# Kernel tuning notes

Hardware: AMD Instinct MI355X
Metric: run time of the kernel (lower is better)

## Reference

```python
import jax, jax.numpy as jnp
import numpy as np
import math

EMBED = 256
HEADS = 8
LEVELS = 4
POINTS = 4
HEAD_DIM = EMBED // HEADS
SHAPES = np.array([[128, 128], [64, 64], [32, 32], [16, 16]], dtype=np.int32)  # (H_l, W_l)


def setup_inputs() -> dict:
    key = jax.random.key(0)
    ks = jax.random.split(key, 8)
    B, N = 2, 10000
    M = int((SHAPES[:, 0] * SHAPES[:, 1]).sum())  # 21760
    query = jax.random.normal(ks[0], (B, N, EMBED), jnp.float32)
    key_t = jax.random.normal(ks[1], (B, M, EMBED), jnp.float32)
    value = jax.random.normal(ks[2], (B, M, EMBED), jnp.float32)
    ref_points = jax.random.uniform(ks[3], (B, N, 1, 2), jnp.float32)  # normalized [0,1]
    spatial_shapes = jnp.asarray(SHAPES)
    starts = np.concatenate([[0], np.cumsum(SHAPES[:, 0] * SHAPES[:, 1])[:-1]]).astype(np.int32)
    level_start_idx = jnp.asarray(starts)
    # sampling_offsets bias: the radial grid init from _reset_parameters
    thetas = np.arange(HEADS, dtype=np.float32) * (2.0 * math.pi / HEADS)
    grid = np.stack([np.cos(thetas), np.sin(thetas)], -1)
    grid = grid / np.abs(grid).max(-1, keepdims=True)
    grid = np.tile(grid[:, None, None, :], (1, LEVELS, POINTS, 1))
    grid = grid * (np.arange(POINTS, dtype=np.float32) + 1.0)[None, None, :, None]
    b_off = jnp.asarray(grid.reshape(-1), jnp.float32)
    W_off = 0.01 * jax.random.normal(ks[4], (EMBED, HEADS * LEVELS * POINTS * 2), jnp.float32)
    W_attn = 0.01 * jax.random.normal(ks[5], (EMBED, HEADS * LEVELS * POINTS), jnp.float32)
    b_attn = jnp.zeros((HEADS * LEVELS * POINTS,), jnp.float32)
    W_v = jax.random.normal(ks[6], (EMBED, EMBED), jnp.float32) / math.sqrt(EMBED)
    b_v = jnp.zeros((EMBED,), jnp.float32)
    return {"query": query, "key": key_t, "value": value, "ref_points": ref_points,
            "spatial_shapes": spatial_shapes, "level_start_idx": level_start_idx,
            "W_off": W_off, "b_off": b_off, "W_attn": W_attn, "b_attn": b_attn,
            "W_v": W_v, "b_v": b_v}


def reference(query, key, value, ref_points, spatial_shapes, level_start_idx,
              W_off, b_off, W_attn, b_attn, W_v, b_v):
    B, N, _ = query.shape
    # value projection, split into heads: (B, M, H, Dh)
    v = (value @ W_v + b_v).reshape(B, -1, HEADS, HEAD_DIM)
    # sampling offsets: (B, N, H, L, P, 2)
    off = (query @ W_off + b_off).reshape(B, N, HEADS, LEVELS, POINTS, 2)
    # attention weights: softmax over L*P
    aw = jax.nn.softmax((query @ W_attn + b_attn).reshape(B, N, HEADS, LEVELS * POINTS), axis=-1)
    aw = aw.reshape(B, N, HEADS, LEVELS, POINTS)
    shapes = np.asarray(spatial_shapes)  # static level shapes
    # normalize offsets per level: x by W_l, y by H_l
    wh = jnp.asarray(shapes[:, ::-1].astype(np.float32))  # (L, 2) = (W, H)
    off = off / wh[None, None, None, :, None, :]
    # K=1 reference point per query -> broadcast add
    locs = ref_points.reshape(B, N, 1, 1, 1, 2) + off  # (B, N, H, L, P, 2) in [0,1]
    starts = np.concatenate([[0], np.cumsum(shapes[:, 0] * shapes[:, 1])])
    b_idx = jnp.arange(B)[:, None, None, None]
    h_idx = jnp.arange(HEADS)[None, None, :, None]
    out = jnp.zeros((B, N, HEADS, HEAD_DIM), v.dtype)
    for l in range(LEVELS):
        Hl, Wl = int(shapes[l, 0]), int(shapes[l, 1])
        v_l = jax.lax.dynamic_slice_in_dim(v, int(starts[l]), Hl * Wl, axis=1)  # (B, Hl*Wl, H, Dh)
        loc = locs[:, :, :, l]  # (B, N, H, P, 2)
        # grid_sample semantics: grid = 2*loc - 1, align_corners=False, zero padding
        x = loc[..., 0] * Wl - 0.5
        y = loc[..., 1] * Hl - 0.5
        x0 = jnp.floor(x)
        y0 = jnp.floor(y)
        lx = x - x0
        ly = y - y0
        x0i = x0.astype(jnp.int32)
        y0i = y0.astype(jnp.int32)
        samp = jnp.zeros(x.shape + (HEAD_DIM,), v.dtype)  # (B, N, H, P, Dh)
        for dy, dx, w in ((0, 0, (1 - lx) * (1 - ly)), (0, 1, lx * (1 - ly)),
                          (1, 0, (1 - lx) * ly), (1, 1, lx * ly)):
            xi = x0i + dx
            yi = y0i + dy
            valid = (xi >= 0) & (xi < Wl) & (yi >= 0) & (yi < Hl)
            idx = jnp.clip(yi, 0, Hl - 1) * Wl + jnp.clip(xi, 0, Wl - 1)
            g = v_l[b_idx, idx, h_idx]  # per-head gather -> (B, N, H, P, Dh)
            samp = samp + jnp.where(valid, w, 0.0)[..., None] * g
        out = out + jnp.einsum('bnhpd,bnhp->bnhd', samp, aw[:, :, :, l])
    return out.reshape(B, N, EMBED)
```

## Files before the change

kernel.cpp:

```cpp
#include <hip/hip_runtime.h>
#include <hip/hip_bf16.h>

#define EMBED    256
#define HEADS    8
#define LEVELS   4
#define POINTS   4
#define BATCH    2
#define M_TOT    21760
#define LDP      (EMBED + 4)

typedef __hip_bfloat16 bf16;
typedef __attribute__((ext_vector_type(8))) short short8;
typedef __attribute__((ext_vector_type(8))) short bf16x8s;
typedef __attribute__((ext_vector_type(4))) float f32x4;

__device__ __constant__ int c_H[LEVELS]  = {128, 64, 32, 16};
__device__ __constant__ int c_St[LEVELS] = {0, 16384, 20480, 21504};

template<bool BF>
__device__ __forceinline__ float ldf(const void* p, size_t i) {
  if (BF) return __bfloat162float(((const bf16*)p)[i]);
  else    return ((const float*)p)[i];
}
__device__ __forceinline__ float vt2f(float x) { return x; }
__device__ __forceinline__ float vt2f(bf16 x)  { return __bfloat162float(x); }

__device__ __forceinline__ void stout(float* p, float v) { *p = v; }
__device__ __forceinline__ void stout(bf16* p, float v)  { *p = __float2bfloat16(v); }
__device__ __forceinline__ void stout_nt(float* p, float v) {
  __builtin_nontemporal_store(v, p);
}
__device__ __forceinline__ void stout_nt(bf16* p, float v)  { *p = __float2bfloat16(v); }

__device__ __forceinline__ void ld2c(const bf16* p, float& lo, float& hi) {
  unsigned u = *(const unsigned*)p;
  lo = __uint_as_float(u << 16);
  hi = __uint_as_float(u & 0xFFFF0000u);
}
__device__ __forceinline__ void ld2c(const float* p, float& lo, float& hi) {
  float2 f = *(const float2*)p;
  lo = f.x; hi = f.y;
}

template<bool BF>
__device__ __forceinline__ float4 ld4(const void* p, size_t i) {
  if (BF) {
    ushort4 u = *(const ushort4*)((const bf16*)p + i);
// ... 16 lines not shown
}

__device__ __forceinline__ void split8(const f32x4 x, const f32x4 y,
                                       bf16x8s& h, bf16x8s& l) {
  float f[8] = {x[0], x[1], x[2], x[3], y[0], y[1], y[2], y[3]};
#pragma unroll
  for (int j = 0; j < 8; ++j) {
    bf16 hb = __float2bfloat16(f[j]);
    float r = f[j] - __bfloat162float(hb);
    bf16 lb = __float2bfloat16(r);
    h[j] = *reinterpret_cast<short*>(&hb);
    l[j] = *reinterpret_cast<short*>(&lb);
  }
}

__global__ __launch_bounds__(256)
void k_detect(const unsigned short* __restrict__ q16, int* __restrict__ flag) {
  __shared__ int cnt;
  if (threadIdx.x == 0) cnt = 0;
  __syncthreads();
  int c = 0;
  for (int i = threadIdx.x; i < 8192; i += 256) {
    unsigned short v = q16[i];
    if ((v & 0x7F80u) == 0x7F80u) ++c;
  }
  if (c) atomicAdd(&cnt, c);
  __syncthreads();
  if (threadIdx.x == 0) flag[0] = (cnt == 0) ? 1 : 0;
}

__global__ __launch_bounds__(256)
void k_transpose_bf16(const unsigned short* __restrict__ W,
                      unsigned short* __restrict__ WT,
                      int K, int N, const int* __restrict__ flag) {
  if (*flag != 1) return;
  __shared__ unsigned short tile[64][65];
  const int ntn = N >> 6;
  const int tk = (int)blockIdx.x / ntn;
  const int tn = (int)blockIdx.x % ntn;
  const int k0 = tk << 6, n0 = tn << 6;
  const int t   = threadIdx.x;
  const int row = t >> 2;
  const int cq  = (t & 3) << 4;
  const unsigned short* src = W + (size_t)(k0 + row) * N + n0 + cq;
#pragma unroll
  for (int j = 0; j < 16; ++j) tile[row][cq + j] = src[j];
  __syncthreads();
  unsigned short* dst = WT + (size_t)(n0 + row) * K + k0 + cq;
#pragma unroll
  for (int j = 0; j < 16; ++j) dst[j] = tile[cq + j][row];
}

__global__ __launch_bounds__(256)
void k_wsplit_all(const float* __restrict__ Wv, const float* __restrict__ Woff,
                  const float* __restrict__ Wattn,
                  bf16* __restrict__ Tvh, bf16* __restrict__ Tvl,
                  bf16* __restrict__ Toh, bf16* __restrict__ Tol,
                  bf16* __restrict__ Tah, bf16* __restrict__ Tal,
                  const int* __restrict__ flag) {
  if (*flag != 0) return;
  int bid = (int)blockIdx.x;
  const float* W; bf16 *H, *L; int N;
  if (bid < 16)      { W = Wv;    H = Tvh; L = Tvl; N = 256; }
  else if (bid < 32) { W = Woff;  H = Toh; L = Tol; N = 256; bid -= 16; }
  else               { W = Wattn; H = Tah; L = Tal; N = 128; bid -= 32; }
  const int K = 256;
  __shared__ float tile[64][65];
  const int ntn = N >> 6;
  const int tk = bid / ntn, tn = bid % ntn;
  const int k0 = tk << 6, n0 = tn << 6;
  const int t   = threadIdx.x;
  const int row = t >> 2;
  const int cq  = (t & 3) << 4;
  const float* src = W + (size_t)(k0 + row) * N + n0 + cq;
#pragma unroll
  for (int j = 0; j < 16; ++j) tile[row][cq + j] = src[j];
  __syncthreads();
  const size_t d0 = (size_t)(n0 + row) * K + k0 + cq;
#pragma unroll
  for (int j = 0; j < 16; ++j) {
    float v = tile[cq + j][row];
    bf16 hb = __float2bfloat16(v);
    float r = v - __bfloat162float(hb);
    H[d0 + j] = hb;
    L[d0 + j] = __float2bfloat16(r);
  }
}

template<class OT>
__global__ __launch_bounds__(256)
void k_mfma_proj(const bf16* __restrict__ A, const bf16* __restrict__ WT,
                 const void* __restrict__ bias, OT* __restrict__ C,
                 int M, int N, const int* __restrict__ flag) {
  if (*flag != 1) return;
  const int colBlocks = N >> 7;
  const int rb = (int)blockIdx.x / colBlocks;
  const int cb = (int)blockIdx.x % colBlocks;
  const int t   = threadIdx.x;
  const int wid = t >> 6;
  const int l   = t & 63;
  const int lrow = l & 15;
  const int lk8  = (l >> 4) << 3;
  const int r0 = rb * 64 + (wid & 1) * 32;
  const int c0 = cb * 128 + (wid >> 1) * 64;

  f32x4 acc[2][4];
#pragma unroll
  for (int rf = 0; rf < 2; ++rf)
#pragma unroll
    for (int cf = 0; cf < 4; ++cf) acc[rf][cf] = (f32x4){0.f, 0.f, 0.f, 0.f};

  const bf16* Ap0 = A + (size_t)min(r0 + lrow,      M - 1) * EMBED + lk8;
// ... 16 lines not shown
    acc[1][1] = __builtin_amdgcn_mfma_f32_16x16x32_bf16(a1, b1, acc[1][1], 0, 0, 0);
    acc[1][2] = __builtin_amdgcn_mfma_f32_16x16x32_bf16(a1, b2, acc[1][2], 0, 0, 0);
    acc[1][3] = __builtin_amdgcn_mfma_f32_16x16x32_bf16(a1, b3, acc[1][3], 0, 0, 0);
  }

  const int rbase = (l >> 4) << 2;
#pragma unroll
  for (int cf = 0; cf < 4; ++cf) {
    const int col = c0 + cf * 16 + lrow;
    const float bv = ldf<true>(bias, col);
#pragma unroll
    for (int rf = 0; rf < 2; ++rf) {
#pragma unroll
      for (int r = 0; r < 4; ++r) {
        const int row = r0 + rf * 16 + rbase + r;
        if (row < M) stout(&C[(size_t)row * N + col], acc[rf][cf][r] + bv);
      }
    }
  }
}

template<int NW, class OT>
__global__ __launch_bounds__(256)
void k_mfma_projf2(const float* __restrict__ A, const bf16* __restrict__ WThi,
                   const bf16* __restrict__ WTlo, const float* __restrict__ bias,
                   OT* __restrict__ C, int M, const int* __restrict__ flag) {
  if (*flag != 0) return;
  constexpr int N = NW * 64;
  const int t   = threadIdx.x;
  const int wid = t >> 6;
  const int l   = t & 63;
  const int lrow = l & 15;
  const int lk8  = (l >> 4) << 3;
  const int r0 = (int)blockIdx.x * 32;
  const int c0 = wid * 64;

  __shared__ float As[32][260];

  constexpr int RPW = 32 / NW;
#pragma unroll
  for (int base = 0; base < RPW; base += 8) {
    f32x4 tmp[8];
#pragma unroll
    for (int i = 0; i < 8; ++i) {
      int r   = wid + (base + i) * NW;
      int row = min(r0 + r, M - 1);
      tmp[i] = __builtin_nontemporal_load(
                 (const f32x4*)(A + (size_t)row * EMBED + (l << 2)));
    }
#pragma unroll
    for (int i = 0; i < 8; ++i) {
      int r = wid + (base + i) * NW;
      *(f32x4*)&As[r][l << 2] = tmp[i];
    }
  }
  __syncthreads();

  f32x4 acc[2][4];
#pragma unroll
  for (int rf = 0; rf < 2; ++rf)
#pragma unroll
    for (int cf = 0; cf < 4; ++cf) acc[rf][cf] = (f32x4){0.f, 0.f, 0.f, 0.f};

  const bf16* Bh = WThi + (size_t)(c0 + lrow) * EMBED + lk8;
  const bf16* Bl = WTlo + (size_t)(c0 + lrow) * EMBED + lk8;

#pragma unroll
  for (int ks = 0; ks < 8; ++ks) {
    const int k = ks * 32;
    bf16x8s a0h, a0l, a1h, a1l;
    split8(*(const f32x4*)&As[lrow     ][k + lk8],
           *(const f32x4*)&As[lrow     ][k + lk8 + 4], a0h, a0l);
    split8(*(const f32x4*)&As[lrow + 16][k + lk8],
           *(const f32x4*)&As[lrow + 16][k + lk8 + 4], a1h, a1l);
    bf16x8s bh0 = *(const bf16x8s*)(Bh + 0 * 16 * EMBED + k);
    bf16x8s bh1 = *(const bf16x8s*)(Bh + 1 * 16 * EMBED + k);
    bf16x8s bh2 = *(const bf16x8s*)(Bh + 2 * 16 * EMBED + k);
    bf16x8s bh3 = *(const bf16x8s*)(Bh + 3 * 16 * EMBED + k);
    bf16x8s bl0 = *(const bf16x8s*)(Bl + 0 * 16 * EMBED + k);
    bf16x8s bl1 = *(const bf16x8s*)(Bl + 1 * 16 * EMBED + k);
// ... 23 lines not shown
    acc[1][1] = __builtin_amdgcn_mfma_f32_16x16x32_bf16(a1l, bh1, acc[1][1], 0, 0, 0);
    acc[1][2] = __builtin_amdgcn_mfma_f32_16x16x32_bf16(a1l, bh2, acc[1][2], 0, 0, 0);
    acc[1][3] = __builtin_amdgcn_mfma_f32_16x16x32_bf16(a1l, bh3, acc[1][3], 0, 0, 0);
  }

  const int rbase = (l >> 4) << 2;
#pragma unroll
  for (int cf = 0; cf < 4; ++cf) {
    const int col = c0 + cf * 16 + lrow;
    const float bv = bias[col];
#pragma unroll
    for (int rf = 0; rf < 2; ++rf) {
#pragma unroll
      for (int r = 0; r < 4; ++r) {
        const int row = r0 + rf * 16 + rbase + r;
        if (row < M) stout_nt(&C[(size_t)row * N + col], acc[rf][cf][r] + bv);
      }
    }
  }
}

template<bool BF>
__device__ __forceinline__ void stage16(const void* __restrict__ A,
                                        float (*rowA)[LDP],
                                        int r0, int M, int t) {
  int r  = t >> 4;
  int rr = min(r0 + r, M - 1);
  int c0 = (t & 15) * 16;
  if (BF) {
    const bf16* ap = (const bf16*)A + (size_t)rr * EMBED + c0;
    short8 a0 = *(const short8*)ap;
// ... 128 lines not shown
template<bool BF, class VT>
__device__ void fused2_body(const void* __restrict__ ref_points,
                            const float* __restrict__ off_pre,
                            const float* __restrict__ scores,
                            const VT* __restrict__ v,
                            void* __restrict__ out, int N, int BN) {
  int q = blockIdx.x;
  if (q >= BN) return;
  int b = q / N;
  int t = threadIdx.x;

  __shared__ float  s_aw[128];
  __shared__ float  s_rp[2];
  __shared__ int4   s_pi[128];
  __shared__ float4 s_pw[128];
  __shared__ float  s_part[2][256];

  if (t < 2)   s_rp[t] = ldf<BF>(ref_points, (size_t)q * 2 + t);
  if (t < 128) s_aw[t] = __builtin_nontemporal_load(&scores[(size_t)q * 128 + t]);
  __syncthreads();

  if (t < 128) {
    int base = t & ~15;
    float mx = -1e30f;
#pragma unroll
    for (int i = 0; i < 16; ++i) mx = fmaxf(mx, s_aw[base + i]);
    float sum = 0.f;
#pragma unroll
    for (int i = 0; i < 16; ++i) sum += expf(s_aw[base + i] - mx);
    float wa = expf(s_aw[t] - mx) / sum;

// ... 61 lines not shown
    oL0 = fmaf(wA.z, lA2, oL0); oH0 = fmaf(wA.z, hA2, oH0);
    oL1 = fmaf(wA.w, lA3, oL1); oH1 = fmaf(wA.w, hA3, oH1);
    oL0 = fmaf(wB.x, lB0, oL0); oH0 = fmaf(wB.x, hB0, oH0);
    oL1 = fmaf(wB.y, lB1, oL1); oH1 = fmaf(wB.y, hB1, oH1);
    oL0 = fmaf(wB.z, lB2, oL0); oH0 = fmaf(wB.z, hB2, oH0);
    oL1 = fmaf(wB.w, lB3, oL1); oH1 = fmaf(wB.w, hB3, oH1);
    oL0 = fmaf(wC.x, lC0, oL0); oH0 = fmaf(wC.x, hC0, oH0);
    oL1 = fmaf(wC.y, lC1, oL1); oH1 = fmaf(wC.y, hC1, oH1);
    oL0 = fmaf(wC.z, lC2, oL0); oH0 = fmaf(wC.z, hC2, oH0);
    oL1 = fmaf(wC.w, lC3, oL1); oH1 = fmaf(wC.w, hC3, oH1);
    oL0 = fmaf(wD.x, lD0, oL0); oH0 = fmaf(wD.x, hD0, oH0);
    oL1 = fmaf(wD.y, lD1, oL1); oH1 = fmaf(wD.y, hD1, oH1);
    oL0 = fmaf(wD.z, lD2, oL0); oH0 = fmaf(wD.z, hD2, oH0);
    oL1 = fmaf(wD.w, lD3, oL1); oH1 = fmaf(wD.w, hD3, oH1);
  }
  s_part[s][ch]     = oL0 + oL1;
  s_part[s][ch + 1] = oH0 + oH1;
  __syncthreads();

  float o = s_part[0][t] + s_part[1][t];
  if (BF) {
    bf16 ob = __float2bfloat16(o);
    __builtin_nontemporal_store(*reinterpret_cast<unsigned short*>(&ob),
                                (unsigned short*)out + (size_t)q * EMBED + t);
  } else {
    __builtin_nontemporal_store(o, (float*)out + (size_t)q * EMBED + t);
  }
}

template<class VT>
__global__ __launch_bounds__(256)
void k_fused2(const void* ref_points, const float* off_pre, const float* scores,
              const VT* v, void* out, int N, int BN, const int* flag) {
  if (*flag) fused2_body<true,  VT>(ref_points, off_pre, scores, v, out, N, BN);
  else       fused2_body<false, VT>(ref_points, off_pre, scores, v, out, N, BN);
}

template<bool BF>
__device__ void vgemv8_body(const void* __restrict__ A, const void* __restrict__ W,
                            const void* __restrict__ bias, float* __restrict__ C,
                            int M) {
  const int t  = threadIdx.x;
  const int r0 = blockIdx.x * 8;
  if (r0 >= M) return;

  __shared__ float rowA[8][EMBED];
  {
    int r  = t >> 5;
    int rr = min(r0 + r, M - 1);
    int c0 = (t & 31) * 8;
// ... 23 lines not shown
  for (int k = 0; k < EMBED; ++k) {
    float w = ldf<BF>(W, (size_t)k * EMBED + n);
#pragma unroll
    for (int r = 0; r < 8; ++r) acc[r] = fmaf(rowA[r][k], w, acc[r]);
  }
#pragma unroll
  for (int r = 0; r < 8; ++r)
    if (r0 + r < M) C[(size_t)(r0 + r) * EMBED + n] = acc[r];
}

__global__ __launch_bounds__(256)
void k_vgemv8(const void* A, const void* W, const void* bias, float* C,
              int M, const int* flag) {
  if (*flag) vgemv8_body<true >(A, W, bias, C, M);
  else       vgemv8_body<false>(A, W, bias, C, M);
}

template<bool BF, class VT>
__device__ void fused_body(const void* __restrict__ query,
                           const void* __restrict__ ref_points,
                           const float* __restrict__ off_pre,
                           const void* __restrict__ W_attn,
                           const void* __restrict__ b_attn,
                           const VT* __restrict__ v,
                           void* __restrict__ out, int N, int BN) {
  int q = blockIdx.x;
  if (q >= BN) return;
  int b = q / N;
  int t = threadIdx.x;

  __shared__ float  row[EMBED];
  __shared__ float  s_part[256];
  __shared__ float  s_aw[HEADS * LEVELS * POINTS];
  __shared__ float  s_rp[2];
  __shared__ int4   s_pi[HEADS * LEVELS * POINTS];
  __shared__ float4 s_pw[HEADS * LEVELS * POINTS];

  row[t] = ldf<BF>(query, (size_t)q * EMBED + t);
  if (t < 2) s_rp[t] = ldf<BF>(ref_points, (size_t)q * 2 + t);
  __syncthreads();

  {
    const int col = t & 127;
    const int e0  = (t >> 7) * 128;
    float acc = 0.f;
#pragma unroll 8
    for (int e = 0; e < 128; ++e)
      acc = fmaf(row[e0 + e], ldf<BF>(W_attn, (size_t)(e0 + e) * 128 + col), acc);
    s_part[t] = acc;
  }
  __syncthreads();
  if (t < 128)
    s_aw[t] = ldf<BF>(b_attn, t) + s_part[t] + s_part[t + 128];
  __syncthreads();

  if (t < 128) {
    int base = t & ~15;
    float mx = -1e30f;
#pragma unroll
    for (int i = 0; i < 16; ++i) mx = fmaxf(mx, s_aw[base + i]);
    float sum = 0.f;
#pragma unroll
    for (int i = 0; i < 16; ++i) sum += expf(s_aw[base + i] - mx);
    float wa = expf(s_aw[t] - mx) / sum;

    int   l  = (t >> 2) & 3;
    int   Wl = 128 >> l;
    float fW = (float)Wl;
    int   st = (int)((65536u - (65536u >> (2 * l))) / 3u);
    float ox = off_pre[(size_t)q * EMBED + 2 * t]     - 0.5f;
    float oy = off_pre[(size_t)q * EMBED + 2 * t + 1] - 0.5f;
    float x = fmaf(s_rp[0], fW, ox);
    float y = fmaf(s_rp[1], fW, oy);
    float x0f = floorf(x), y0f = floorf(y);
    float lx = x - x0f, ly = y - y0f;
    int x0 = (int)x0f, y0 = (int)y0f;
    int x1 = x0 + 1,   y1 = y0 + 1;
    float w00 = wa * (1.f - lx) * (1.f - ly);
    float w01 = wa * lx * (1.f - ly);
    float w10 = wa * (1.f - lx) * ly;
    float w11 = wa * lx * ly;
    bool vx0 = (unsigned)x0 < (unsigned)Wl;
    bool vx1 = (unsigned)x1 < (unsigned)Wl;
    bool vy0 = (unsigned)y0 < (unsigned)Wl;
    bool vy1 = (unsigned)y1 < (unsigned)Wl;
    int xc0 = min(max(x0, 0), Wl - 1), xc1 = min(max(x1, 0), Wl - 1);
    int yc0 = min(max(y0, 0), Wl - 1), yc1 = min(max(y1, 0), Wl - 1);
    int r0i = st + yc0 * Wl;
    int r1i = st + yc1 * Wl;
    int4 pi; float4 pw;
    pi.x = (r0i + xc0) << 8;  pw.x = (vx0 && vy0) ? w00 : 0.f;
    pi.y = (r0i + xc1) << 8;  pw.y = (vx1 && vy0) ? w01 : 0.f;
    pi.z = (r1i + xc0) << 8;  pw.z = (vx0 && vy1) ? w10 : 0.f;
    pi.w = (r1i + xc1) << 8;  pw.w = (vx1 && vy1) ? w11 : 0.f;
    s_pi[t] = pi;
    s_pw[t] = pw;
  }
  __syncthreads();

  const int h = t >> 5;
  const VT* vbt = v + (size_t)b * M_TOT * EMBED + t;
  float o = 0.f;
#pragma unroll
  for (int lp = 0; lp < 16; ++lp) {
    int c = (h << 4) + lp;
    int4   i4 = s_pi[c];
    float4 w4 = s_pw[c];
    o = fmaf(w4.x, vt2f(vbt[i4.x]), o);
    o = fmaf(w4.y, vt2f(vbt[i4.y]), o);
    o = fmaf(w4.z, vt2f(vbt[i4.z]), o);
    o = fmaf(w4.w, vt2f(vbt[i4.w]), o);
  }
  if (BF) ((bf16*)out)[(size_t)q * EMBED + t] = __float2bfloat16(o);
  else    ((float*)out)[(size_t)q * EMBED + t] = o;
}

template<class VT>
__global__ __launch_bounds__(256)
void k_fused(const void* query, const void* ref_points, const float* off_pre,
             const void* W_attn, const void* b_attn,
             const VT* v, void* out, int N, int BN, const int* flag) {
  if (*flag) fused_body<true,  VT>(query, ref_points, off_pre, W_attn, b_attn, v, out, N, BN);
  else       fused_body<false, VT>(query, ref_points, off_pre, W_attn, b_attn, v, out, N, BN);
}

template<bool BF, class VT>
__device__ void vproj_body(const void* __restrict__ value,
                           const void* __restrict__ W_v,
                           const void* __restrict__ b_v,
                           VT* __restrict__ v, int BM) {
  int m = blockIdx.x;
  if (m >= BM) return;
  int t = threadIdx.x;
  __shared__ float row[EMBED];
  row[t] = ldf<BF>(value, (size_t)m * EMBED + t);
  __syncthreads();
  float acc = ldf<BF>(b_v, t);
#pragma unroll 8
  for (int e = 0; e < EMBED; ++e)
    acc = fmaf(row[e], ldf<BF>(W_v, (size_t)e * EMBED + t), acc);
  if (sizeof(VT) == 2) ((bf16*)v)[(size_t)m * EMBED + t] = __float2bfloat16(acc);
  else                 ((float*)v)[(size_t)m * EMBED + t] = acc;
}

template<class VT>
__global__ __launch_bounds__(256)
void k_value_proj(const void* value, const void* W_v, const void* b_v,
                  VT* v, int BM, const int* flag) {
  if (*flag) vproj_body<true,  VT>(value, W_v, b_v, v, BM);
  else       vproj_body<false, VT>(value, W_v, b_v, v, BM);
}

template<bool BF, class VT>
__device__ void fusedfb_body(const void* __restrict__ query,
                             const void* __restrict__ ref_points,
                             const void* __restrict__ W_off,
                             const void* __restrict__ b_off,
                             const void* __restrict__ W_attn,
                             const void* __restrict__ b_attn,
                             const VT* __restrict__ v,
                             void* __restrict__ out, int N, int BN) {
  int q = blockIdx.x;
  if (q >= BN) return;
  int b = q / N;
  int t = threadIdx.x;
// ... 73 lines not shown
  }
  if (BF) ((bf16*)out)[(size_t)q * EMBED + t] = __float2bfloat16(o);
  else    ((float*)out)[(size_t)q * EMBED + t] = o;
}

template<class VT>
__global__ __launch_bounds__(256)
void k_fused_fb(const void* query, const void* ref_points,
                const void* W_off, const void* b_off,
                const void* W_attn, const void* b_attn,
                const VT* v, void* out, int N, int BN, const int* flag) {
  if (*flag) fusedfb_body<true,  VT>(query, ref_points, W_off, b_off, W_attn, b_attn, v, out, N, BN);
  else       fusedfb_body<false, VT>(query, ref_points, W_off, b_off, W_attn, b_attn, v, out, N, BN);
}

extern "C" void kernel_launch(void* const* d_in, const int* in_sizes, int n_in,
                              void* d_out, int out_size, void* d_ws, size_t ws_size,
                              hipStream_t stream) {
  const void* query      = d_in[0];
  const void* value      = d_in[2];
  const void* ref_points = d_in[3];
  const void* W_off  = d_in[6];
  const void* b_off  = d_in[7];
  const void* W_attn = d_in[8];
  const void* b_attn = d_in[9];
  const void* W_v    = d_in[10];
  const void* b_v    = d_in[11];

  const int BN = in_sizes[0] / EMBED;
  const int BM = in_sizes[2] / EMBED;
  const int N  = BN / BATCH;

  int*  flag    = (int*)d_ws;
  char* ws_base = (char*)d_ws + 256;

  k_detect<<<1, 256, 0, stream>>>((const unsigned short*)query, flag);

  const size_t sz_v    = (size_t)BM * EMBED * sizeof(float);
  const size_t sz_off  = (size_t)BN * EMBED * sizeof(float);
  const size_t sz_attn = (size_t)BN * 128 * sizeof(float);
  const size_t sz_T    = (size_t)(256 * 256 * 2 + 256 * 128) * 2  * 2;
  const size_t need_mfma = 256 + sz_v + sz_off + sz_attn + sz_T;
  const size_t need_full = 256 + sz_v + sz_off + sz_attn;
  const size_t need_mid  = 256 + sz_v + sz_off;

  if (ws_size >= need_mfma) {
    bf16*  ws_v    = (bf16*)ws_base;
    float* ws_off  = (float*)(ws_base + sz_v);
    float* ws_attn = (float*)(ws_base + sz_v + sz_off);
    unsigned short* wsT = (unsigned short*)(ws_base + sz_v + sz_off + sz_attn);
    unsigned short* wsT_v    = wsT;
    unsigned short* wsT_off  = wsT + 256 * 256;
    unsigned short* wsT_attn = wsT + 2 * 256 * 256;
    bf16* Tvh = (bf16*)wsT;
    bf16* Tvl = Tvh + 256 * 256;
    bf16* Toh = Tvl + 256 * 256;
    bf16* Tol = Toh + 256 * 256;
    bf16* Tah = Tol + 256 * 256;
    bf16* Tal = Tah + 256 * 128;

    const int rbV64 = (BM + 63) / 64;
    const int rbQ64 = (BN + 63) / 64;
    k_transpose_bf16<<<16, 256, 0, stream>>>((const unsigned short*)W_v,    wsT_v,    256, 256, flag);
    k_transpose_bf16<<<16, 256, 0, stream>>>((const unsigned short*)W_off,  wsT_off,  256, 256, flag);
    k_transpose_bf16<<< 8, 256, 0, stream>>>((const unsigned short*)W_attn, wsT_attn, 256, 128, flag);
    k_mfma_proj<bf16 ><<<rbV64 * 2, 256, 0, stream>>>((const bf16*)value, (const bf16*)wsT_v,
                                                      b_v, ws_v, BM, 256, flag);
    k_mfma_proj<float><<<rbQ64 * 2, 256, 0, stream>>>((const bf16*)query, (const bf16*)wsT_off,
                                                      b_off, ws_off, BN, 256, flag);
    k_mfma_proj<float><<<rbQ64,     256, 0, stream>>>((const bf16*)query, (const bf16*)wsT_attn,
                                                      b_attn, ws_attn, BN, 128, flag);

    const int gV32 = (BM + 31) / 32;
    const int gQ32 = (BN + 31) / 32;
    k_wsplit_all<<<40, 256, 0, stream>>>((const float*)W_v, (const float*)W_off,
                                         (const float*)W_attn,
                                         Tvh, Tvl, Toh, Tol, Tah, Tal, flag);
    k_mfma_projf2<4, bf16 ><<<gV32, 256, 0, stream>>>((const float*)value, Tvh, Tvl,
                                                      (const float*)b_v, ws_v, BM, flag);
    k_mfma_projf2<4, float><<<gQ32, 256, 0, stream>>>((const float*)query, Toh, Tol,
                                                      (const float*)b_off, ws_off, BN, flag);
    k_mfma_projf2<2, float><<<gQ32, 128, 0, stream>>>((const float*)query, Tah, Tal,
                                                      (const float*)b_attn, ws_attn, BN, flag);

    k_fused2<bf16><<<BN, 256, 0, stream>>>(ref_points, ws_off, ws_attn, ws_v,
                                           d_out, N, BN, flag);
  } else if (ws_size >= need_full) {
    float* ws_v    = (float*)ws_base;
    float* ws_off  = (float*)(ws_base + sz_v);
    float* ws_attn = (float*)(ws_base + sz_v + sz_off);
    k_vgemv4x4<<<(BM + 15) / 16, 256, 0, stream>>>(value, W_v, b_v, ws_v, BM, flag);
    k_vgemv4x4<<<(BN + 15) / 16, 256, 0, stream>>>(query, W_off, b_off, ws_off, BN, flag);
    k_agemv4<<<(BN + 15) / 16, 256, 0, stream>>>(query, W_attn, b_attn, ws_attn, BN, flag);
    k_fused2<float><<<BN, 256, 0, stream>>>(ref_points, ws_off, ws_attn, ws_v,
                                            d_out, N, BN, flag);
  } else if (ws_size >= need_mid) {
    float* ws_v   = (float*)ws_base;
    float* ws_off = (float*)(ws_base + sz_v);
    k_vgemv8<<<(BM + 7) / 8, 256, 0, stream>>>(value, W_v, b_v, ws_v, BM, flag);
    k_vgemv8<<<(BN + 7) / 8, 256, 0, stream>>>(query, W_off, b_off, ws_off, BN, flag);
    k_fused<float><<<BN, 256, 0, stream>>>(query, ref_points, ws_off,
                                           W_attn, b_attn, ws_v, d_out, N, BN, flag);
  } else {
    bf16* ws_v = (bf16*)ws_base;
    k_value_proj<bf16><<<BM, 256, 0, stream>>>(value, W_v, b_v, ws_v, BM, flag);
    k_fused_fb<bf16><<<BN, 256, 0, stream>>>(query, ref_points, W_off, b_off,
                                             W_attn, b_attn, ws_v, d_out, N, BN, flag);
  }
}
```

Before: 317.5 us.

## Merge detect/transpose/split and projection launches into fewer combined kernels

Folds dtype detection into an 80-block prep kernel that also performs the bf16 weight transpose or the fp32 hi/lo split, so every block detects redundantly and skips the branch it does not need. The three bf16 projection GEMMs and the three fp32 split-precision GEMMs each become a single launch that routes work segments by block index. This cuts the launch count from about eleven to four on the main path, reducing launch gaps and tail underutilisation. The cost is redundant detection reads in every prep block and idle waves in the attention segment, which now uses 256-thread blocks with half the waves exiting early. It also changes the fused kernel's partial-sum shared layout and removes the unused mid-size fallback path.

New measurement: 287.5 us. 1.1x faster.

```diff
diff --git a/kernel.cpp b/kernel.cpp
--- a/kernel.cpp
+++ b/kernel.cpp
@@ -27,10 +27,6 @@
 
 __device__ __forceinline__ void stout(float* p, float v) { *p = v; }
 __device__ __forceinline__ void stout(bf16* p, float v)  { *p = __float2bfloat16(v); }
-__device__ __forceinline__ void stout_nt(float* p, float v) {
-  __builtin_nontemporal_store(v, p);
-}
-__device__ __forceinline__ void stout_nt(bf16* p, float v)  { *p = __float2bfloat16(v); }
 
 __device__ __forceinline__ void ld2c(const bf16* p, float& lo, float& hi) {
   unsigned u = *(const unsigned*)p;
@@ -77,88 +73,111 @@
   }
 }
 
-__global__ __launch_bounds__(256)
-void k_detect(const unsigned short* __restrict__ q16, int* __restrict__ flag) {
-  __shared__ int cnt;
-  if (threadIdx.x == 0) cnt = 0;
+__device__ __forceinline__ int block_detect(const unsigned short* q16, int t,
+                                            int* cnt) {
+  if (t == 0) *cnt = 0;
   __syncthreads();
   int c = 0;
-  for (int i = threadIdx.x; i < 8192; i += 256) {
+  for (int i = t; i < 8192; i += 256) {
     unsigned short v = q16[i];
     if ((v & 0x7F80u) == 0x7F80u) ++c;
   }
-  if (c) atomicAdd(&cnt, c);
-  __syncthreads();
-  if (threadIdx.x == 0) flag[0] = (cnt == 0) ? 1 : 0;
+  if (c) atomicAdd(cnt, c);
+  __syncthreads();
+  return (*cnt == 0) ? 1 : 0;
 }
 
 __global__ __launch_bounds__(256)
-void k_transpose_bf16(const unsigned short* __restrict__ W,
-                      unsigned short* __restrict__ WT,
-                      int K, int N, const int* __restrict__ flag) {
-  if (*flag != 1) return;
-  __shared__ unsigned short tile[64][65];
-  const int ntn = N >> 6;
-  const int tk = (int)blockIdx.x / ntn;
-  const int tn = (int)blockIdx.x % ntn;
-  const int k0 = tk << 6, n0 = tn << 6;
-  const int t   = threadIdx.x;
+void k_prep(const unsigned short* __restrict__ q16, int* __restrict__ flag,
+            const void* __restrict__ Wv, const void* __restrict__ Woff,
+            const void* __restrict__ Wattn,
+            unsigned short* __restrict__ wsT_v,
+            unsigned short* __restrict__ wsT_off,
+            unsigned short* __restrict__ wsT_attn,
+            bf16* __restrict__ Tvh, bf16* __restrict__ Tvl,
+            bf16* __restrict__ Toh, bf16* __restrict__ Tol,
+            bf16* __restrict__ Tah, bf16* __restrict__ Tal) {
+  __shared__ int cnt;
+  __shared__ float  ftile[64][65];
+  __shared__ unsigned short stile[64][65];
+
+  const int t = threadIdx.x;
+  const int isbf = block_detect(q16, t, &cnt);
+  if ((int)blockIdx.x == 0 && t == 0) flag[0] = isbf;
+
   const int row = t >> 2;
   const int cq  = (t & 3) << 4;
-  const unsigned short* src = W + (size_t)(k0 + row) * N + n0 + cq;
-#pragma unroll
-  for (int j = 0; j < 16; ++j) tile[row][cq + j] = src[j];
-  __syncthreads();
-  unsigned short* dst = WT + (size_t)(n0 + row) * K + k0 + cq;
-#pragma unroll
-  for (int j = 0; j < 16; ++j) dst[j] = tile[cq + j][row];
+  const int K = 256;
+
+  if ((int)blockIdx.x < 40) {
+    if (isbf) return;
+    int bid = (int)blockIdx.x;
+    const float* W; bf16 *H, *L; int N;
+    if (bid < 16)      { W = (const float*)Wv;    H = Tvh; L = Tvl; N = 256; }
+    else if (bid < 32) { W = (const float*)Woff;  H = Toh; L = Tol; N = 256; bid -= 16; }
+    else               { W = (const float*)Wattn; H = Tah; L = Tal; N = 128; bid -= 32; }
+    const int ntn = N >> 6;
+    const int tk = bid / ntn, tn = bid % ntn;
+    const int k0 = tk << 6, n0 = tn << 6;
+    const float* src = W + (size_t)(k0 + row) * N + n0 + cq;
+#pragma unroll
+    for (int j = 0; j < 16; ++j) ftile[row][cq + j] = src[j];
+    __syncthreads();
+    const size_t d0 = (size_t)(n0 + row) * K + k0 + cq;
+#pragma unroll
+    for (int j = 0; j < 16; ++j) {
+      float v = ftile[cq + j][row];
+      bf16 hb = __float2bfloat16(v);
+      float r = v - __bfloat162float(hb);
+      H[d0 + j] = hb;
+      L[d0 + j] = __float2bfloat16(r);
+    }
+  } else {
+    if (!isbf) return;
+    int bid = (int)blockIdx.x - 40;
+    const unsigned short* W; unsigned short* WT; int N;
+    if (bid < 16)      { W = (const unsigned short*)Wv;    WT = wsT_v;    N = 256; }
+    else if (bid < 32) { W = (const unsigned short*)Woff;  WT = wsT_off;  N = 256; bid -= 16; }
+    else               { W = (const unsigned short*)Wattn; WT = wsT_attn; N = 128; bid -= 32; }
+    const int ntn = N >> 6;
+    const int tk = bid / ntn, tn = bid % ntn;
+    const int k0 = tk << 6, n0 = tn << 6;
+    const unsigned short* src = W + (size_t)(k0 + row) * N + n0 + cq;
+#pragma unroll
+    for (int j = 0; j < 16; ++j) stile[row][cq + j] = src[j];
+    __syncthreads();
+    unsigned short* dst = WT + (size_t)(n0 + row) * K + k0 + cq;
+#pragma unroll
+    for (int j = 0; j < 16; ++j) dst[j] = stile[cq + j][row];
+  }
 }
 
 __global__ __launch_bounds__(256)
-void k_wsplit_all(const float* __restrict__ Wv, const float* __restrict__ Woff,
-                  const float* __restrict__ Wattn,
-                  bf16* __restrict__ Tvh, bf16* __restrict__ Tvl,
-                  bf16* __restrict__ Toh, bf16* __restrict__ Tol,
-                  bf16* __restrict__ Tah, bf16* __restrict__ Tal,
-                  const int* __restrict__ flag) {
-  if (*flag != 0) return;
+void k_proj_all(const bf16* __restrict__ value, const bf16* __restrict__ query,
+                const unsigned short* __restrict__ wsT_v,
+                const unsigned short* __restrict__ wsT_off,
+                const unsigned short* __restrict__ wsT_attn,
+                const void* __restrict__ b_v, const void* __restrict__ b_off,
+                const void* __restrict__ b_attn,
+                bf16* __restrict__ Cv, float* __restrict__ Coff,
+                float* __restrict__ Cattn,
+                int BM, int BN, int g0, int g1,
+                const int* __restrict__ flag) {
+  if (*flag != 1) return;
   int bid = (int)blockIdx.x;
-  const float* W; bf16 *H, *L; int N;
-  if (bid < 16)      { W = Wv;    H = Tvh; L = Tvl; N = 256; }
-  else if (bid < 32) { W = Woff;  H = Toh; L = Tol; N = 256; bid -= 16; }
-  else               { W = Wattn; H = Tah; L = Tal; N = 128; bid -= 32; }
-  const int K = 256;
-  __shared__ float tile[64][65];
-  const int ntn = N >> 6;
-  const int tk = bid / ntn, tn = bid % ntn;
-  const int k0 = tk << 6, n0 = tn << 6;
-  const int t   = threadIdx.x;
-  const int row = t >> 2;
-  const int cq  = (t & 3) << 4;
-  const float* src = W + (size_t)(k0 + row) * N + n0 + cq;
-#pragma unroll
-  for (int j = 0; j < 16; ++j) tile[row][cq + j] = src[j];
-  __syncthreads();
-  const size_t d0 = (size_t)(n0 + row) * K + k0 + cq;
-#pragma unroll
-  for (int j = 0; j < 16; ++j) {
-    float v = tile[cq + j][row];
-    bf16 hb = __float2bfloat16(v);
-    float r = v - __bfloat162float(hb);
-    H[d0 + j] = hb;
-    L[d0 + j] = __float2bfloat16(r);
-  }
-}
-
-template<class OT>
-__global__ __launch_bounds__(256)
-void k_mfma_proj(const bf16* __restrict__ A, const bf16* __restrict__ WT,
-                 const void* __restrict__ bias, OT* __restrict__ C,
-                 int M, int N, const int* __restrict__ flag) {
-  if (*flag != 1) return;
+  int seg, sb;
+  if (bid < g0)            { seg = 0; sb = bid; }
+  else if (bid < g0 + g1)  { seg = 1; sb = bid - g0; }
+  else                     { seg = 2; sb = bid - g0 - g1; }
+
+  const bf16* A; const bf16* WT; const void* bias; int M, N;
+  if (seg == 0)      { A = value; WT = (const bf16*)wsT_v;    bias = b_v;    M = BM; N = 256; }
+  else if (seg == 1) { A = query; WT = (const bf16*)wsT_off;  bias = b_off;  M = BN; N = 256; }
+  else               { A = query; WT = (const bf16*)wsT_attn; bias = b_attn; M = BN; N = 128; }
+
   const int colBlocks = N >> 7;
-  const int rb = (int)blockIdx.x / colBlocks;
-  const int cb = (int)blockIdx.x % colBlocks;
+  const int rb = sb / colBlocks;
+  const int cb = sb % colBlocks;
   const int t   = threadIdx.x;
   const int wid = t >> 6;
   const int l   = t & 63;
@@ -205,56 +224,80 @@
 #pragma unroll
       for (int r = 0; r < 4; ++r) {
         const int row = r0 + rf * 16 + rbase + r;
-        if (row < M) stout(&C[(size_t)row * N + col], acc[rf][cf][r] + bv);
+        if (row < M) {
+          float o = acc[rf][cf][r] + bv;
+          size_t idx = (size_t)row * N + col;
+          if (seg == 0)      Cv[idx]   = __float2bfloat16(o);
+          else if (seg == 1) Coff[idx] = o;
+          else               Cattn[idx] = o;
+        }
       }
     }
   }
 }
 
-template<int NW, class OT>
 __global__ __launch_bounds__(256)
-void k_mfma_projf2(const float* __restrict__ A, const bf16* __restrict__ WThi,
-                   const bf16* __restrict__ WTlo, const float* __restrict__ bias,
-                   OT* __restrict__ C, int M, const int* __restrict__ flag) {
+void k_projf2_all(const float* __restrict__ value, const float* __restrict__ query,
+                  const bf16* __restrict__ Tvh, const bf16* __restrict__ Tvl,
+                  const bf16* __restrict__ Toh, const bf16* __restrict__ Tol,
+                  const bf16* __restrict__ Tah, const bf16* __restrict__ Tal,
+                  const float* __restrict__ b_v, const float* __restrict__ b_off,
+                  const float* __restrict__ b_attn,
+                  bf16* __restrict__ Cv, float* __restrict__ Coff,
+                  float* __restrict__ Cattn,
+                  int BM, int BN, int gV, int gQ,
+                  const int* __restrict__ flag) {
   if (*flag != 0) return;
-  constexpr int N = NW * 64;
+  int bid = (int)blockIdx.x;
+  int seg, rblk;
+  if (bid < gV)           { seg = 0; rblk = bid; }
+  else if (bid < gV + gQ) { seg = 1; rblk = bid - gV; }
+  else                    { seg = 2; rblk = bid - gV - gQ; }
+
+  const float* A; const bf16 *Bh0, *Bl0; const float* bias; int M, N;
+  if (seg == 0)      { A = value; Bh0 = Tvh; Bl0 = Tvl; bias = b_v;    M = BM; N = 256; }
+  else if (seg == 1) { A = query; Bh0 = Toh; Bl0 = Tol; bias = b_off;  M = BN; N = 256; }
+  else               { A = query; Bh0 = Tah; Bl0 = Tal; bias = b_attn; M = BN; N = 128; }
+
   const int t   = threadIdx.x;
   const int wid = t >> 6;
   const int l   = t & 63;
   const int lrow = l & 15;
   const int lk8  = (l >> 4) << 3;
-  const int r0 = (int)blockIdx.x * 32;
+  const int r0 = rblk * 32;
   const int c0 = wid * 64;
+  const bool active = (seg != 2) || (wid < 2);
 
   __shared__ float As[32][260];
 
-  constexpr int RPW = 32 / NW;
-#pragma unroll
-  for (int base = 0; base < RPW; base += 8) {
+#pragma unroll
+  for (int base = 0; base < 8; base += 8) {
     f32x4 tmp[8];
 #pragma unroll
     for (int i = 0; i < 8; ++i) {
-      int r   = wid + (base + i) * NW;
+      int r   = wid + (base + i) * 4;
       int row = min(r0 + r, M - 1);
       tmp[i] = __builtin_nontemporal_load(
                  (const f32x4*)(A + (size_t)row * EMBED + (l << 2)));
     }
 #pragma unroll
     for (int i = 0; i < 8; ++i) {
-      int r = wid + (base + i) * NW;
+      int r = wid + (base + i) * 4;
       *(f32x4*)&As[r][l << 2] = tmp[i];
     }
   }
   __syncthreads();
 
+  if (!active) return;
+
   f32x4 acc[2][4];
 #pragma unroll
   for (int rf = 0; rf < 2; ++rf)
 #pragma unroll
     for (int cf = 0; cf < 4; ++cf) acc[rf][cf] = (f32x4){0.f, 0.f, 0.f, 0.f};
 
-  const bf16* Bh = WThi + (size_t)(c0 + lrow) * EMBED + lk8;
-  const bf16* Bl = WTlo + (size_t)(c0 + lrow) * EMBED + lk8;
+  const bf16* Bh = Bh0 + (size_t)(c0 + lrow) * EMBED + lk8;
+  const bf16* Bl = Bl0 + (size_t)(c0 + lrow) * EMBED + lk8;
 
 #pragma unroll
   for (int ks = 0; ks < 8; ++ks) {
@@ -308,7 +351,13 @@
 #pragma unroll
       for (int r = 0; r < 4; ++r) {
         const int row = r0 + rf * 16 + rbase + r;
-        if (row < M) stout_nt(&C[(size_t)row * N + col], acc[rf][cf][r] + bv);
+        if (row < M) {
+          float o = acc[rf][cf][r] + bv;
+          size_t idx = (size_t)row * N + col;
+          if (seg == 0)      Cv[idx] = __float2bfloat16(o);
+          else if (seg == 1) __builtin_nontemporal_store(o, &Coff[idx]);
+          else               __builtin_nontemporal_store(o, &Cattn[idx]);
+        }
       }
     }
   }
@@ -467,7 +516,7 @@
   __shared__ float  s_rp[2];
   __shared__ int4   s_pi[128];
   __shared__ float4 s_pw[128];
-  __shared__ float  s_part[2][256];
+  __shared__ float  s_part[2][2][128];
 
   if (t < 2)   s_rp[t] = ldf<BF>(ref_points, (size_t)q * 2 + t);
   if (t < 128) s_aw[t] = __builtin_nontemporal_load(&scores[(size_t)q * 128 + t]);
@@ -559,11 +608,11 @@
     oL0 = fmaf(wD.z, lD2, oL0); oH0 = fmaf(wD.z, hD2, oH0);
     oL1 = fmaf(wD.w, lD3, oL1); oH1 = fmaf(wD.w, hD3, oH1);
   }
-  s_part[s][ch]     = oL0 + oL1;
-  s_part[s][ch + 1] = oH0 + oH1;
-  __syncthreads();
-
-  float o = s_part[0][t] + s_part[1][t];
+  s_part[s][0][c] = oL0 + oL1;
+  s_part[s][1][c] = oH0 + oH1;
+  __syncthreads();
+
+  float o = s_part[0][t & 1][t >> 1] + s_part[1][t & 1][t >> 1];
   if (BF) {
     bf16 ob = __float2bfloat16(o);
     __builtin_nontemporal_store(*reinterpret_cast<unsigned short*>(&ob),
@@ -579,6 +628,13 @@
               const VT* v, void* out, int N, int BN, const int* flag) {
   if (*flag) fused2_body<true,  VT>(ref_points, off_pre, scores, v, out, N, BN);
   else       fused2_body<false, VT>(ref_points, off_pre, scores, v, out, N, BN);
+}
+
+__global__ __launch_bounds__(256)
+void k_detect(const unsigned short* __restrict__ q16, int* __restrict__ flag) {
+  __shared__ int cnt;
+  int isbf = block_detect(q16, threadIdx.x, &cnt);
+  if (threadIdx.x == 0) flag[0] = isbf;
 }
 
 template<bool BF>
@@ -632,141 +688,6 @@
               int M, const int* flag) {
   if (*flag) vgemv8_body<true >(A, W, bias, C, M);
   else       vgemv8_body<false>(A, W, bias, C, M);
-}
-
-template<bool BF, class VT>
-__device__ void fused_body(const void* __restrict__ query,
-                           const void* __restrict__ ref_points,
-                           const float* __restrict__ off_pre,
-                           const void* __restrict__ W_attn,
-                           const void* __restrict__ b_attn,
-                           const VT* __restrict__ v,
-                           void* __restrict__ out, int N, int BN) {
-  int q = blockIdx.x;
-  if (q >= BN) return;
-  int b = q / N;
-  int t = threadIdx.x;
-
-  __shared__ float  row[EMBED];
-  __shared__ float  s_part[256];
-  __shared__ float  s_aw[HEADS * LEVELS * POINTS];
-  __shared__ float  s_rp[2];
-  __shared__ int4   s_pi[HEADS * LEVELS * POINTS];
-  __shared__ float4 s_pw[HEADS * LEVELS * POINTS];
-
-  row[t] = ldf<BF>(query, (size_t)q * EMBED + t);
-  if (t < 2) s_rp[t] = ldf<BF>(ref_points, (size_t)q * 2 + t);
-  __syncthreads();
-
-  {
-    const int col = t & 127;
-    const int e0  = (t >> 7) * 128;
-    float acc = 0.f;
-#pragma unroll 8
-    for (int e = 0; e < 128; ++e)
-      acc = fmaf(row[e0 + e], ldf<BF>(W_attn, (size_t)(e0 + e) * 128 + col), acc);
-    s_part[t] = acc;
-  }
-  __syncthreads();
-  if (t < 128)
-    s_aw[t] = ldf<BF>(b_attn, t) + s_part[t] + s_part[t + 128];
-  __syncthreads();
-
-  if (t < 128) {
-    int base = t & ~15;
-    float mx = -1e30f;
-#pragma unroll
-    for (int i = 0; i < 16; ++i) mx = fmaxf(mx, s_aw[base + i]);
-    float sum = 0.f;
-#pragma unroll
-    for (int i = 0; i < 16; ++i) sum += expf(s_aw[base + i] - mx);
-    float wa = expf(s_aw[t] - mx) / sum;
-
-    int   l  = (t >> 2) & 3;
-    int   Wl = 128 >> l;
-    float fW = (float)Wl;
-    int   st = (int)((65536u - (65536u >> (2 * l))) / 3u);
-    float ox = off_pre[(size_t)q * EMBED + 2 * t]     - 0.5f;
-    float oy = off_pre[(size_t)q * EMBED + 2 * t + 1] - 0.5f;
-    float x = fmaf(s_rp[0], fW, ox);
-    float y = fmaf(s_rp[1], fW, oy);
-    float x0f = floorf(x), y0f = floorf(y);
-    float lx = x - x0f, ly = y - y0f;
-    int x0 = (int)x0f, y0 = (int)y0f;
-    int x1 = x0 + 1,   y1 = y0 + 1;
-    float w00 = wa * (1.f - lx) * (1.f - ly);
-    float w01 = wa * lx * (1.f - ly);
-    float w10 = wa * (1.f - lx) * ly;
-    float w11 = wa * lx * ly;
-    bool vx0 = (unsigned)x0 < (unsigned)Wl;
-    bool vx1 = (unsigned)x1 < (unsigned)Wl;
-    bool vy0 = (unsigned)y0 < (unsigned)Wl;
-    bool vy1 = (unsigned)y1 < (unsigned)Wl;
-    int xc0 = min(max(x0, 0), Wl - 1), xc1 = min(max(x1, 0), Wl - 1);
-    int yc0 = min(max(y0, 0), Wl - 1), yc1 = min(max(y1, 0), Wl - 1);
-    int r0i = st + yc0 * Wl;
-    int r1i = st + yc1 * Wl;
-    int4 pi; float4 pw;
-    pi.x = (r0i + xc0) << 8;  pw.x = (vx0 && vy0) ? w00 : 0.f;
-    pi.y = (r0i + xc1) << 8;  pw.y = (vx1 && vy0) ? w01 : 0.f;
-    pi.z = (r1i + xc0) << 8;  pw.z = (vx0 && vy1) ? w10 : 0.f;
-    pi.w = (r1i + xc1) << 8;  pw.w = (vx1 && vy1) ? w11 : 0.f;
-    s_pi[t] = pi;
-    s_pw[t] = pw;
-  }
-  __syncthreads();
-
-  const int h = t >> 5;
-  const VT* vbt = v + (size_t)b * M_TOT * EMBED + t;
-  float o = 0.f;
-#pragma unroll
-  for (int lp = 0; lp < 16; ++lp) {
-    int c = (h << 4) + lp;
-    int4   i4 = s_pi[c];
-    float4 w4 = s_pw[c];
-    o = fmaf(w4.x, vt2f(vbt[i4.x]), o);
-    o = fmaf(w4.y, vt2f(vbt[i4.y]), o);
-    o = fmaf(w4.z, vt2f(vbt[i4.z]), o);
-    o = fmaf(w4.w, vt2f(vbt[i4.w]), o);
-  }
-  if (BF) ((bf16*)out)[(size_t)q * EMBED + t] = __float2bfloat16(o);
-  else    ((float*)out)[(size_t)q * EMBED + t] = o;
-}
-
-template<class VT>
-__global__ __launch_bounds__(256)
-void k_fused(const void* query, const void* ref_points, const float* off_pre,
-             const void* W_attn, const void* b_attn,
-             const VT* v, void* out, int N, int BN, const int* flag) {
-  if (*flag) fused_body<true,  VT>(query, ref_points, off_pre, W_attn, b_attn, v, out, N, BN);
-  else       fused_body<false, VT>(query, ref_points, off_pre, W_attn, b_attn, v, out, N, BN);
-}
-
-template<bool BF, class VT>
-__device__ void vproj_body(const void* __restrict__ value,
-                           const void* __restrict__ W_v,
-                           const void* __restrict__ b_v,
-                           VT* __restrict__ v, int BM) {
-  int m = blockIdx.x;
-  if (m >= BM) return;
-  int t = threadIdx.x;
-  __shared__ float row[EMBED];
-  row[t] = ldf<BF>(value, (size_t)m * EMBED + t);
-  __syncthreads();
-  float acc = ldf<BF>(b_v, t);
-#pragma unroll 8
-  for (int e = 0; e < EMBED; ++e)
-    acc = fmaf(row[e], ldf<BF>(W_v, (size_t)e * EMBED + t), acc);
-  if (sizeof(VT) == 2) ((bf16*)v)[(size_t)m * EMBED + t] = __float2bfloat16(acc);
-  else                 ((float*)v)[(size_t)m * EMBED + t] = acc;
-}
-
-template<class VT>
-__global__ __launch_bounds__(256)
-void k_value_proj(const void* value, const void* W_v, const void* b_v,
-                  VT* v, int BM, const int* flag) {
-  if (*flag) vproj_body<true,  VT>(value, W_v, b_v, v, BM);
-  else       vproj_body<false, VT>(value, W_v, b_v, v, BM);
 }
 
 template<bool BF, class VT>
@@ -870,6 +791,33 @@
   else       fusedfb_body<false, VT>(query, ref_points, W_off, b_off, W_attn, b_attn, v, out, N, BN);
 }
 
+template<bool BF, class VT>
+__device__ void vproj_body(const void* __restrict__ value,
+                           const void* __restrict__ W_v,
+                           const void* __restrict__ b_v,
+                           VT* __restrict__ v, int BM) {
+  int m = blockIdx.x;
+  if (m >= BM) return;
+  int t = threadIdx.x;
+  __shared__ float row[EMBED];
+  row[t] = ldf<BF>(value, (size_t)m * EMBED + t);
+  __syncthreads();
+  float acc = ldf<BF>(b_v, t);
+#pragma unroll 8
+  for (int e = 0; e < EMBED; ++e)
+    acc = fmaf(row[e], ldf<BF>(W_v, (size_t)e * EMBED + t), acc);
+  if (sizeof(VT) == 2) ((bf16*)v)[(size_t)m * EMBED + t] = __float2bfloat16(acc);
+  else                 ((float*)v)[(size_t)m * EMBED + t] = acc;
+}
+
+template<class VT>
+__global__ __launch_bounds__(256)
+void k_value_proj(const void* value, const void* W_v, const void* b_v,
+                  VT* v, int BM, const int* flag) {
+  if (*flag) vproj_body<true,  VT>(value, W_v, b_v, v, BM);
+  else       vproj_body<false, VT>(value, W_v, b_v, v, BM);
+}
+
 extern "C" void kernel_launch(void* const* d_in, const int* in_sizes, int n_in,
                               void* d_out, int out_size, void* d_ws, size_t ws_size,
                               hipStream_t stream) {
@@ -890,12 +838,10 @@
   int*  flag    = (int*)d_ws;
   char* ws_base = (char*)d_ws + 256;
 
-  k_detect<<<1, 256, 0, stream>>>((const unsigned short*)query, flag);
-
   const size_t sz_v    = (size_t)BM * EMBED * sizeof(float);
   const size_t sz_off  = (size_t)BN * EMBED * sizeof(float);
   const size_t sz_attn = (size_t)BN * 128 * sizeof(float);
-  const size_t sz_T    = (size_t)(256 * 256 * 2 + 256 * 128) * 2  * 2;
+  const size_t sz_T    = (size_t)(256 * 256 * 2 + 256 * 128) * 2 * 2;
   const size_t need_mfma = 256 + sz_v + sz_off + sz_attn + sz_T;
   const size_t need_full = 256 + sz_v + sz_off + sz_attn;
   const size_t need_mid  = 256 + sz_v + sz_off;
@@ -917,48 +863,38 @@
 
     const int rbV64 = (BM + 63) / 64;
     const int rbQ64 = (BN + 63) / 64;
-    k_transpose_bf16<<<16, 256, 0, stream>>>((const unsigned short*)W_v,    wsT_v,    256, 256, flag);
-    k_transpose_bf16<<<16, 256, 0, stream>>>((const unsigned short*)W_off,  wsT_off,  256, 256, flag);
-    k_transpose_bf16<<< 8, 256, 0, stream>>>((const unsigned short*)W_attn, wsT_attn, 256, 128, flag);
-    k_mfma_proj<bf16 ><<<rbV64 * 2, 256, 0, stream>>>((const bf16*)value, (const bf16*)wsT_v,
-                                                      b_v, ws_v, BM, 256, flag);
-    k_mfma_proj<float><<<rbQ64 * 2, 256, 0, stream>>>((const bf16*)query, (const bf16*)wsT_off,
-                                                      b_off, ws_off, BN, 256, flag);
-    k_mfma_proj<float><<<rbQ64,     256, 0, stream>>>((const bf16*)query, (const bf16*)wsT_attn,
-                                                      b_attn, ws_attn, BN, 128, flag);
-
+    const int g0 = rbV64 * 2, g1 = rbQ64 * 2, g2 = rbQ64;
     const int gV32 = (BM + 31) / 32;
     const int gQ32 = (BN + 31) / 32;
-    k_wsplit_all<<<40, 256, 0, stream>>>((const float*)W_v, (const float*)W_off,
-                                         (const float*)W_attn,
-                                         Tvh, Tvl, Toh, Tol, Tah, Tal, flag);
-    k_mfma_projf2<4, bf16 ><<<gV32, 256, 0, stream>>>((const float*)value, Tvh, Tvl,
-                                                      (const float*)b_v, ws_v, BM, flag);
-    k_mfma_projf2<4, float><<<gQ32, 256, 0, stream>>>((const float*)query, Toh, Tol,
-                                                      (const float*)b_off, ws_off, BN, flag);
-    k_mfma_projf2<2, float><<<gQ32, 128, 0, stream>>>((const float*)query, Tah, Tal,
-                                                      (const float*)b_attn, ws_attn, BN, flag);
-
+
+    k_prep<<<80, 256, 0, stream>>>((const unsigned short*)query, flag,
+                                   W_v, W_off, W_attn,
+                                   wsT_v, wsT_off, wsT_attn,
+                                   Tvh, Tvl, Toh, Tol, Tah, Tal);
+    k_proj_all<<<g0 + g1 + g2, 256, 0, stream>>>(
+        (const bf16*)value, (const bf16*)query,
+        wsT_v, wsT_off, wsT_attn, b_v, b_off, b_attn,
+        ws_v, ws_off, ws_attn, BM, BN, g0, g1, flag);
+    k_projf2_all<<<gV32 + 2 * gQ32, 256, 0, stream>>>(
+        (const float*)value, (const float*)query,
+        Tvh, Tvl, Toh, Tol, Tah, Tal,
+        (const float*)b_v, (const float*)b_off, (const float*)b_attn,
+        ws_v, ws_off, ws_attn, BM, BN, gV32, gQ32, flag);
     k_fused2<bf16><<<BN, 256, 0, stream>>>(ref_points, ws_off, ws_attn, ws_v,
                                            d_out, N, BN, flag);
   } else if (ws_size >= need_full) {
     float* ws_v    = (float*)ws_base;
     float* ws_off  = (float*)(ws_base + sz_v);
     float* ws_attn = (float*)(ws_base + sz_v + sz_off);
+    k_detect<<<1, 256, 0, stream>>>((const unsigned short*)query, flag);
     k_vgemv4x4<<<(BM + 15) / 16, 256, 0, stream>>>(value, W_v, b_v, ws_v, BM, flag);
     k_vgemv4x4<<<(BN + 15) / 16, 256, 0, stream>>>(query, W_off, b_off, ws_off, BN, flag);
     k_agemv4<<<(BN + 15) / 16, 256, 0, stream>>>(query, W_attn, b_attn, ws_attn, BN, flag);
     k_fused2<float><<<BN, 256, 0, stream>>>(ref_points, ws_off, ws_attn, ws_v,
                                             d_out, N, BN, flag);
-  } else if (ws_size >= need_mid) {
-    float* ws_v   = (float*)ws_base;
-    float* ws_off = (float*)(ws_base + sz_v);
-    k_vgemv8<<<(BM + 7) / 8, 256, 0, stream>>>(value, W_v, b_v, ws_v, BM, flag);
-    k_vgemv8<<<(BN + 7) / 8, 256, 0, stream>>>(query, W_off, b_off, ws_off, BN, flag);
-    k_fused<float><<<BN, 256, 0, stream>>>(query, ref_points, ws_off,
-                                           W_attn, b_attn, ws_v, d_out, N, BN, flag);
   } else {
     bf16* ws_v = (bf16*)ws_base;
+    k_detect<<<1, 256, 0, stream>>>((const unsigned short*)query, flag);
     k_value_proj<bf16><<<BM, 256, 0, stream>>>(value, W_v, b_v, ws_v, BM, flag);
     k_fused_fb<bf16><<<BN, 256, 0, stream>>>(query, ref_points, W_off, b_off,
                                              W_attn, b_attn, ws_v, d_out, N, BN, flag);
```
